# Optimization experiments

Measured on AMD Instinct MI355X. Metric: run time of the kernel, lower is better.

## Reference

```python
import jax, jax.numpy as jnp
import numpy as np

D_IN, D_ATT = 48, 8

def setup_inputs() -> dict:
    key = jax.random.key(0)
    k0, k1, k2, k3, k4 = jax.random.split(key, 5)
    N = 1048576
    x = jax.random.normal(k0, (N, D_IN), dtype=jnp.float32)
    # torch Linear weights have shape [out_features, in_features]
    Wk = jax.random.normal(k1, (D_ATT, D_IN), dtype=jnp.float32) * 0.1
    Wq = jax.random.normal(k2, (D_ATT, D_IN), dtype=jnp.float32) * 0.1
    Wv = jax.random.normal(k3, (D_ATT, D_IN), dtype=jnp.float32) * 0.1
    Wo = jax.random.normal(k4, (D_IN, D_ATT), dtype=jnp.float32) * 0.1
    return {"x": x, "Wk": Wk, "Wq": Wq, "Wv": Wv, "Wo": Wo}

def reference(x, Wk, Wq, Wv, Wo):
    # q, k, v: [N, 8]
    k = x @ Wk.T
    q = x @ Wq.T
    v = x @ Wv.T
    # attn: [8, 8] = q^T k / sqrt(8), softmax over dim=1 (columns)
    scores = (q.T @ k) / jnp.sqrt(jnp.float32(D_ATT))
    attn = jax.nn.softmax(scores, axis=1)
    # pre_output: [N, 8]; output: [N, 48]
    pre = v @ attn
    return pre @ Wo.T
```

## Files before the change

### kernel.cpp

```cpp
#include <hip/hip_runtime.h>
#include <hip/hip_bf16.h>


#define DI 48

typedef __attribute__((ext_vector_type(8))) short short8;
typedef __attribute__((ext_vector_type(4))) float f32x4;

__device__ inline unsigned int pack_bf16(float lo, float hi) {
  __hip_bfloat162 h = __float22bfloat162_rn(make_float2(lo, hi));
  return *reinterpret_cast<unsigned int*>(&h);
}

constexpr int GB1 = 1024;
constexpr int GB2 = 2048;
constexpr int NC  = 32;
constexpr int SDT = 20;
constexpr int SDR = 28;
constexpr int WDW = 48 * SDT + 32 * SDR;

__global__ __launch_bounds__(256) void k_gram_v(const float* __restrict__ x,
                                                const float* __restrict__ Wv,
                                                float* __restrict__ G,
                                                __hip_bfloat16* __restrict__ v,
                                                int N) {
  __shared__ unsigned int sh[4 * WDW];
  const int tid = threadIdx.x;
  const int wave = tid >> 6, lane = tid & 63;
  unsigned int* xt = &sh[wave * WDW];
  unsigned int* xr = xt + 48 * SDT;
  const int quad = lane >> 4, m = lane & 15;

  short8 wv0 = {}, wv1 = {};
  if (m < 8) {
    const float* wrow = Wv + m * DI + 8 * quad;
    float4 c0 = *(const float4*)(wrow);
    float4 c1 = *(const float4*)(wrow + 4);
    unsigned int u0[4] = { pack_bf16(c0.x, c0.y), pack_bf16(c0.z, c0.w),
                           pack_bf16(c1.x, c1.y), pack_bf16(c1.z, c1.w) };
    wv0 = *(const short8*)u0;
    if (quad < 2) {
      float4 d0 = *(const float4*)(wrow + 32);
      float4 d1 = *(const float4*)(wrow + 36);
      unsigned int u1[4] = { pack_bf16(d0.x, d0.y), pack_bf16(d0.z, d0.w),
                             pack_bf16(d1.x, d1.y), pack_bf16(d1.z, d1.w) };
      wv1 = *(const short8*)u1;
    }
  }

  f32x4 acc[3][3] = {};

  const int rows_per_block = N / GB1;
  const int rows_per_wave = rows_per_block >> 2;
  const long long base0 = (long long)blockIdx.x * rows_per_block + wave * rows_per_wave;

  auto LOADT = [&](int tile, float4* va, float4* vb) {
#pragma unroll
    for (int s = 0; s < 3; ++s) {
      int task = lane + 64 * s;
      int rp = task / 12, cg = task % 12;
      const float4* p = (const float4*)(x + (base0 + tile * 32 + 2 * rp) * DI) + cg;
      va[s] = p[0];
      vb[s] = *(const float4*)((const float*)p + DI);
    }
  };

  auto PROCESS = [&](int tile, const float4* va, const float4* vb) {
    const long long rowt = base0 + (long long)tile * 32;
#pragma unroll
    for (int s = 0; s < 3; ++s) {
      int task = lane + 64 * s;
      int rp = task / 12, cg = task % 12;
      int c0 = 4 * cg;
      xt[(c0 + 0) * SDT + rp] = pack_bf16(va[s].x, vb[s].x);
      xt[(c0 + 1) * SDT + rp] = pack_bf16(va[s].y, vb[s].y);
      xt[(c0 + 2) * SDT + rp] = pack_bf16(va[s].z, vb[s].z);
      xt[(c0 + 3) * SDT + rp] = pack_bf16(va[s].w, vb[s].w);
      unsigned int ra[2] = { pack_bf16(va[s].x, va[s].y), pack_bf16(va[s].z, va[s].w) };
      unsigned int rb[2] = { pack_bf16(vb[s].x, vb[s].y), pack_bf16(vb[s].z, vb[s].w) };
      *(uint2*)&xr[(2 * rp) * SDR + 2 * cg]     = *(const uint2*)ra;
      *(uint2*)&xr[(2 * rp + 1) * SDR + 2 * cg] = *(const uint2*)rb;
    }
    asm volatile("s_waitcnt lgkmcnt(0)" ::: "memory");
    short8 f[3];
#pragma unroll
    for (int t = 0; t < 3; ++t)
      f[t] = *(const short8*)&xt[(16 * t + m) * SDT + quad * 4];
#pragma unroll
    for (int i = 0; i < 3; ++i)
#pragma unroll
      for (int j = 0; j < 3; ++j)
        acc[i][j] = __builtin_amdgcn_mfma_f32_16x16x32_bf16(f[i], f[j], acc[i][j], 0, 0, 0);
#pragma unroll
    for (int g = 0; g < 2; ++g) {
      short8 a0 = *(const short8*)&xr[(16 * g + m) * SDR + quad * 4];
      short8 a1 = {};
      if (quad < 2) a1 = *(const short8*)&xr[(16 * g + m) * SDR + 16 + quad * 4];
      f32x4 vg = {};
      vg = __builtin_amdgcn_mfma_f32_16x16x32_bf16(a0, wv0, vg, 0, 0, 0);
      vg = __builtin_amdgcn_mfma_f32_16x16x32_bf16(a1, wv1, vg, 0, 0, 0);
      if (m < 8) {
        __hip_bfloat16* vr = v + (rowt + 16 * g + 4 * quad) * 8 + m;
#pragma unroll
        for (int r = 0; r < 4; ++r) vr[r * 8] = __float2bfloat16(vg[r]);
      }
    }
  };

  float4 vaA[3], vbA[3], vaB[3], vbB[3];
  LOADT(0, vaA, vbA);
#pragma unroll
  for (int t = 0; t < 8; t += 2) {
    if (t + 1 < 8) LOADT(t + 1, vaB, vbB);
    PROCESS(t, vaA, vbA);
    if (t + 2 < 8) LOADT(t + 2, vaA, vbA);
    if (t + 1 < 8) PROCESS(t + 1, vaB, vbB);
  }

  __syncthreads();
  float* red = (float*)sh;
  if (wave >= 2) {
    float* dst = red + (wave - 2) * 2304 + lane * 36;
#pragma unroll
    for (int i = 0; i < 3; ++i)
#pragma unroll
      for (int j = 0; j < 3; ++j)
#pragma unroll
        for (int r = 0; r < 4; ++r) dst[(i * 3 + j) * 4 + r] = acc[i][j][r];
  }
  __syncthreads();
  if (wave < 2) {
    const float* s2 = red + wave * 2304 + lane * 36;
#pragma unroll
    for (int i = 0; i < 3; ++i)
#pragma unroll
      for (int j = 0; j < 3; ++j)
#pragma unroll
        for (int r = 0; r < 4; ++r) acc[i][j][r] += s2[(i * 3 + j) * 4 + r];
  }
  __syncthreads();
  if (wave == 1) {
    float* dst = red + lane * 36;
#pragma unroll
    for (int i = 0; i < 3; ++i)
#pragma unroll
      for (int j = 0; j < 3; ++j)
#pragma unroll
        for (int r = 0; r < 4; ++r) dst[(i * 3 + j) * 4 + r] = acc[i][j][r];
  }
  __syncthreads();
  if (wave == 0) {
    const float* s1 = red + lane * 36;
    float* Gp = G + (blockIdx.x & (NC - 1)) * 2304;
#pragma unroll
    for (int i = 0; i < 3; ++i)
#pragma unroll
      for (int j = 0; j < 3; ++j)
#pragma unroll
        for (int r = 0; r < 4; ++r) {
          float val = acc[i][j][r] + s1[(i * 3 + j) * 4 + r];
          atomicAdd(&Gp[(16 * i + quad * 4 + r) * 48 + 16 * j + m], val);
        }
  }
}

__global__ void k_combine(const float* __restrict__ G,
                          const float* __restrict__ Wk,
                          const float* __restrict__ Wq,
                          const float* __restrict__ Wo,
                          __hip_bfloat16* __restrict__ Mt2) {
  __shared__ float sG[2304];
  __shared__ float sWk[384], sWq[384], sWo[384];
  __shared__ float sU[384];
  __shared__ float sA[64];
  const int t = threadIdx.x;

  for (int i = t; i < 2304; i += 256) {
    float s = 0.f;
#pragma unroll
    for (int c = 0; c < NC; ++c) s += G[c * 2304 + i];
    sG[i] = s;
  }
  for (int i = t; i < 384; i += 256) {
    sWk[i] = Wk[i]; sWq[i] = Wq[i]; sWo[i] = Wo[i];
  }
  __syncthreads();

  for (int e = t; e < 384; e += 256) {
    int q = e & 7, i = e >> 3;
    float s = 0.f;
#pragma unroll
    for (int j = 0; j < 48; ++j) s += sG[i * 48 + j] * sWk[q * 48 + j];
    sU[q * 48 + i] = s;
  }
  __syncthreads();

  if (t < 64) {
    int p = t >> 3;
    float s = 0.f;
#pragma unroll
    for (int i = 0; i < 48; ++i) s += sWq[p * 48 + i] * sU[(t & 7) * 48 + i];
    s *= 0.35355339059327373f;
    float mx = s;
    for (int d = 1; d < 8; d <<= 1) mx = fmaxf(mx, __shfl_xor(mx, d));
    float e = expf(s - mx);
    float den = e;
    for (int d = 1; d < 8; d <<= 1) den += __shfl_xor(den, d);
    sA[t] = e / den;
  }
  __syncthreads();

  for (int e = t; e < 384; e += 256) {
    int p = e & 7, col = e >> 3;
    float s = 0.f;
#pragma unroll
    for (int q = 0; q < 8; ++q) s += sA[p * 8 + q] * sWo[col * 8 + q];
    Mt2[col * 8 + p] = __float2bfloat16(s);
  }
}

__global__ __launch_bounds__(256) void k_out_v(const __hip_bfloat16* __restrict__ v,
                                               const __hip_bfloat16* __restrict__ Mt2,
                                               float* __restrict__ out, int N) {
  const int tid = threadIdx.x;
  const int wave = tid >> 6, lane = tid & 63;
  const int quad = lane >> 4, m = lane & 15;

  short8 b[3] = {short8{}, short8{}, short8{}};
  if (quad == 0) {
#pragma unroll
    for (int t = 0; t < 3; ++t)
      b[t] = *(const short8*)(Mt2 + (16 * t + m) * 8);
  }

  const int rows_per_block = N / GB2;
  const int rows_per_wave = rows_per_block >> 2;
  const int ng = rows_per_wave >> 4;
  const long long base = (long long)blockIdx.x * rows_per_block + wave * rows_per_wave;

  for (int g = 0; g < ng; ++g) {
    const long long rowg = base + (long long)g * 16;
    short8 af = {};
    if (quad == 0) af = *(const short8*)(v + (rowg + m) * 8);
    f32x4 acc[3] = {};
#pragma unroll
    for (int t = 0; t < 3; ++t)
      acc[t] = __builtin_amdgcn_mfma_f32_16x16x32_bf16(b[t], af, acc[t], 0, 0, 0);
    float* orow = out + rowg * DI;
#pragma unroll
    for (int t = 0; t < 3; ++t)
      *(float4*)(orow + m * DI + 16 * t + 4 * quad) = *(const float4*)&acc[t];
  }
}

extern "C" void kernel_launch(void* const* d_in, const int* in_sizes, int n_in,
                              void* d_out, int out_size, void* d_ws, size_t ws_size,
                              hipStream_t stream) {
  const float* x  = (const float*)d_in[0];
  const float* Wk = (const float*)d_in[1];
  const float* Wq = (const float*)d_in[2];
  const float* Wv = (const float*)d_in[3];
  const float* Wo = (const float*)d_in[4];
  float* out = (float*)d_out;
  const int N = in_sizes[0] / DI;

  float* G = (float*)d_ws;
  __hip_bfloat16* Mt2 = (__hip_bfloat16*)((char*)d_ws + 294912);
  __hip_bfloat16* v   = (__hip_bfloat16*)((char*)d_ws + 307200);

  hipMemsetAsync(G, 0, NC * 2304 * sizeof(float), stream);
  k_gram_v<<<GB1, 256, 0, stream>>>(x, Wv, G, v, N);
  k_combine<<<1, 256, 0, stream>>>(G, Wk, Wq, Wo, Mt2);
  k_out_v<<<GB2, 256, 0, stream>>>(v, Mt2, out, N);
}
```

Before: 384.4 us.

## Fuse combine step into output kernel and drop partitioned Gram accumulators

Removes the single-block combine kernel: each output block now recomputes the tiny attention/Wo product from the Gram matrix in shared memory before its MFMA loop. The 32-way partitioned Gram buffers are collapsed into one 48x48 buffer, so all 1024 blocks atomically add into the same addresses. This saves one kernel launch and the serial single-block stage. In exchange, every one of 2048 blocks redundantly recomputes the small matrices, and atomic contention on the Gram buffer rises.

```diff
diff --git a/kernel.cpp b/kernel.cpp
--- a/kernel.cpp
+++ b/kernel.cpp
@@ -14,7 +14,6 @@
 
 constexpr int GB1 = 1024;
 constexpr int GB2 = 2048;
-constexpr int NC  = 32;
 constexpr int SDT = 20;
 constexpr int SDR = 28;
 constexpr int WDW = 48 * SDT + 32 * SDR;
@@ -151,7 +150,6 @@
   __syncthreads();
   if (wave == 0) {
     const float* s1 = red + lane * 36;
-    float* Gp = G + (blockIdx.x & (NC - 1)) * 2304;
 #pragma unroll
     for (int i = 0; i < 3; ++i)
 #pragma unroll
@@ -159,34 +157,32 @@
 #pragma unroll
         for (int r = 0; r < 4; ++r) {
           float val = acc[i][j][r] + s1[(i * 3 + j) * 4 + r];
-          atomicAdd(&Gp[(16 * i + quad * 4 + r) * 48 + 16 * j + m], val);
+          atomicAdd(&G[(16 * i + quad * 4 + r) * 48 + 16 * j + m], val);
         }
   }
 }
 
-__global__ void k_combine(const float* __restrict__ G,
-                          const float* __restrict__ Wk,
-                          const float* __restrict__ Wq,
-                          const float* __restrict__ Wo,
-                          __hip_bfloat16* __restrict__ Mt2) {
+__global__ __launch_bounds__(256) void k_out_v(const __hip_bfloat16* __restrict__ v,
+                                               const float* __restrict__ G,
+                                               const float* __restrict__ Wk,
+                                               const float* __restrict__ Wq,
+                                               const float* __restrict__ Wo,
+                                               float* __restrict__ out, int N) {
   __shared__ float sG[2304];
   __shared__ float sWk[384], sWq[384], sWo[384];
   __shared__ float sU[384];
   __shared__ float sA[64];
-  const int t = threadIdx.x;
-
-  for (int i = t; i < 2304; i += 256) {
-    float s = 0.f;
-#pragma unroll
-    for (int c = 0; c < NC; ++c) s += G[c * 2304 + i];
-    sG[i] = s;
-  }
-  for (int i = t; i < 384; i += 256) {
+  __shared__ __hip_bfloat16 sMt[384];
+  const int tid = threadIdx.x;
+  const int wave = tid >> 6, lane = tid & 63;
+  const int quad = lane >> 4, m = lane & 15;
+
+  for (int i = tid; i < 2304; i += 256) sG[i] = G[i];
+  for (int i = tid; i < 384; i += 256) {
     sWk[i] = Wk[i]; sWq[i] = Wq[i]; sWo[i] = Wo[i];
   }
   __syncthreads();
-
-  for (int e = t; e < 384; e += 256) {
+  for (int e = tid; e < 384; e += 256) {
     int q = e & 7, i = e >> 3;
     float s = 0.f;
 #pragma unroll
@@ -194,43 +190,34 @@
     sU[q * 48 + i] = s;
   }
   __syncthreads();
-
-  if (t < 64) {
-    int p = t >> 3;
+  if (tid < 64) {
+    int p = tid >> 3;
     float s = 0.f;
 #pragma unroll
-    for (int i = 0; i < 48; ++i) s += sWq[p * 48 + i] * sU[(t & 7) * 48 + i];
+    for (int i = 0; i < 48; ++i) s += sWq[p * 48 + i] * sU[(tid & 7) * 48 + i];
     s *= 0.35355339059327373f;
     float mx = s;
     for (int d = 1; d < 8; d <<= 1) mx = fmaxf(mx, __shfl_xor(mx, d));
     float e = expf(s - mx);
     float den = e;
     for (int d = 1; d < 8; d <<= 1) den += __shfl_xor(den, d);
-    sA[t] = e / den;
-  }
-  __syncthreads();
-
-  for (int e = t; e < 384; e += 256) {
+    sA[tid] = e / den;
+  }
+  __syncthreads();
+  for (int e = tid; e < 384; e += 256) {
     int p = e & 7, col = e >> 3;
     float s = 0.f;
 #pragma unroll
     for (int q = 0; q < 8; ++q) s += sA[p * 8 + q] * sWo[col * 8 + q];
-    Mt2[col * 8 + p] = __float2bfloat16(s);
-  }
-}
-
-__global__ __launch_bounds__(256) void k_out_v(const __hip_bfloat16* __restrict__ v,
-                                               const __hip_bfloat16* __restrict__ Mt2,
-                                               float* __restrict__ out, int N) {
-  const int tid = threadIdx.x;
-  const int wave = tid >> 6, lane = tid & 63;
-  const int quad = lane >> 4, m = lane & 15;
+    sMt[col * 8 + p] = __float2bfloat16(s);
+  }
+  __syncthreads();
 
   short8 b[3] = {short8{}, short8{}, short8{}};
   if (quad == 0) {
 #pragma unroll
     for (int t = 0; t < 3; ++t)
-      b[t] = *(const short8*)(Mt2 + (16 * t + m) * 8);
+      b[t] = *(const short8*)(&sMt[(16 * t + m) * 8]);
   }
 
   const int rows_per_block = N / GB2;
@@ -265,11 +252,9 @@
   const int N = in_sizes[0] / DI;
 
   float* G = (float*)d_ws;
-  __hip_bfloat16* Mt2 = (__hip_bfloat16*)((char*)d_ws + 294912);
-  __hip_bfloat16* v   = (__hip_bfloat16*)((char*)d_ws + 307200);
-
-  hipMemsetAsync(G, 0, NC * 2304 * sizeof(float), stream);
+  __hip_bfloat16* v = (__hip_bfloat16*)((char*)d_ws + 16384);
+
+  hipMemsetAsync(G, 0, 2304 * sizeof(float), stream);
   k_gram_v<<<GB1, 256, 0, stream>>>(x, Wv, G, v, N);
-  k_combine<<<1, 256, 0, stream>>>(G, Wk, Wq, Wo, Mt2);
-  k_out_v<<<GB2, 256, 0, stream>>>(v, Mt2, out, N);
-}
+  k_out_v<<<GB2, 256, 0, stream>>>(v, G, Wk, Wq, Wo, out, N);
+}
```

After: 377.3 us. About the same (-1.8%).
